# Optimization experiments

Measured on AMD Instinct MI355X. Metric: run time of the kernel, lower is better.

The kernel has to match this reference:

```python
import jax, jax.numpy as jnp
import numpy as np

I = 512   # input_size
H = 512   # hidden_size
Z = 0.1   # zoneout rate (eval-mode deterministic blend)
S = 128   # number of segments
B = 64    # batch


def setup_inputs() -> dict:
    rng = np.random.default_rng(0)
    durs = rng.integers(4, 13, size=(S, B)).astype(np.int64)  # [S, B], all >= 1
    T = int(durs.sum(0).max())
    key = jax.random.key(0)
    k0, k1, k2, k3, k4 = jax.random.split(key, 5)
    k = 1.0 / np.sqrt(H)
    x = jax.random.normal(k0, (T, B, I), jnp.float32)
    W_ih = jax.random.uniform(k1, (4 * H, I), jnp.float32, -k, k)
    W_hh = jax.random.uniform(k2, (4 * H, H), jnp.float32, -k, k)
    b_ih = jax.random.uniform(k3, (4 * H,), jnp.float32, -k, k)
    b_hh = jax.random.uniform(k4, (4 * H,), jnp.float32, -k, k)
    return {"x": x, "durs": jnp.asarray(durs), "W_ih": W_ih, "W_hh": W_hh,
            "b_ih": b_ih, "b_hh": b_hh}


def _duration_masks(durs, T):
    # durs: [S, B] -> per-batch segment-end (reset) frame indices and masks
    durs_bs = durs.T                                   # [B, S]
    reset_idx = jnp.cumsum(durs_bs, axis=1) - 1        # [B, S] last frame of each segment
    mel_lengths = jnp.sum(durs_bs, axis=1)             # [B]
    t = jnp.arange(T)
    reset_mask = jnp.any(t[None, :, None] == reset_idx[:, None, :], axis=-1)  # [B, T]
    valid = t[None, :] < mel_lengths[:, None]          # [B, T] frames within mel length
    retain = (~reset_mask) & valid                     # state kept where not reset/pad
    return reset_idx, retain.T, valid.T                # retain/valid as [T, B]


def reference(x, durs, W_ih, W_hh, b_ih, b_hh):
    T, Bb, _ = x.shape
    reset_idx, retain, valid = _duration_masks(durs, T)
    # Precompute the input contribution to the gates for all timesteps (one big GEMM)
    xg = jnp.einsum('tbi,gi->tbg', x, W_ih) + b_ih + b_hh   # [T, B, 4H]
    retain_f = retain.astype(x.dtype)                       # [T, B]

    def step(carry, inp):
        h, c = carry
        xg_t, retain_t = inp
        gates = xg_t + h @ W_hh.T                           # [B, 4H]
        i, f, g, o = jnp.split(gates, 4, axis=-1)           # torch LSTMCell order i,f,g,o
        i = jax.nn.sigmoid(i); f = jax.nn.sigmoid(f); o = jax.nn.sigmoid(o)
        g = jnp.tanh(g)
        c_new = f * c + i * g
        h_new = o * jnp.tanh(c_new)
        # eval-mode zoneout: deterministic blend with previous state
        h_z = Z * h + (1.0 - Z) * h_new
        c_z = Z * c + (1.0 - Z) * c_new
        m = retain_t[:, None]                               # zero state at segment resets / padding
        return (h_z * m, c_z * m), h_z

    h0 = jnp.zeros((Bb, H), x.dtype)
    (h, c), outputs = jax.lax.scan(step, (h0, h0), (xg, retain_f))
    outputs = outputs * valid[:, :, None].astype(outputs.dtype)  # [T, B, H]
    # segout: hidden state at each segment's last frame -> [B, S, H]
    segout = jnp.take_along_axis(outputs.transpose(1, 0, 2), reset_idx[:, :, None], axis=1)
    return outputs, h, c, segout
```

## Files before the change

kernel.cpp:

```cpp
#include <hip/hip_runtime.h>
#include <hip/hip_fp16.h>

#define IDIM 512
#define HDIM 512
#define NGATE 2048
#define SEGS 128
#define BATCH 64
#define ZK 0.1f

typedef _Float16 f16;
typedef _Float16 f16x8 __attribute__((ext_vector_type(8)));
typedef float f32x4 __attribute__((ext_vector_type(4)));

__device__ __forceinline__ void gload16(const void* g, void* l) {
  __builtin_amdgcn_global_load_lds((const __attribute__((address_space(1))) void*)g,
                                   (__attribute__((address_space(3))) void*)l, 16, 0, 0);
}
__device__ __forceinline__ float sigmoidf_(float x) { return 1.0f / (1.0f + __expf(-x)); }
__device__ __forceinline__ float tanhf_(float x) { return 2.0f / (1.0f + __expf(-2.0f * x)) - 1.0f; }

__global__ void prep_kernel(const int* __restrict__ durs, int4* __restrict__ meta,
                            int* __restrict__ Mk, int* __restrict__ mel) {
  __shared__ int hist[16];
  __shared__ int cur[16];
  int tid = threadIdx.x;
  if (tid < 16) hist[tid] = 0;
  __syncthreads();
  int b = tid;
  for (int s = 0; s < SEGS; ++s) {
    int d = durs[s * BATCH + b] & 15;
    atomicAdd(&hist[d], 1);
  }
  __syncthreads();
  if (tid == 0) {
    int run = 0;
    for (int d = 15; d >= 0; --d) { cur[d] = run; run += hist[d]; }
    for (int kk = 0; kk < 12; ++kk) Mk[kk] = cur[kk];
  }
  __syncthreads();
  int run = 0;
  for (int s = 0; s < SEGS; ++s) {
    int d = durs[s * BATCH + b] & 15;
    int pos = atomicAdd(&cur[d], 1);
    meta[pos] = make_int4(run, b, s, d);
    run += d;
  }
  mel[b] = run;
}

__global__ void wprep_kernel(const float* __restrict__ Wih, const float* __restrict__ Whh,
                             const float* __restrict__ bih, const float* __restrict__ bhh,
                             f16* __restrict__ Wc, float* __restrict__ biasp) {
  int n = blockIdx.x;
  int G = n >> 6, q = (n >> 4) & 3, r = n & 15;
  int j = G * 16 + r;
  int orig = q * 512 + j;
  for (int kk = threadIdx.x; kk < 1024; kk += blockDim.x) {
    float v = (kk < 512) ? Wih[(size_t)orig * 512 + kk] : Whh[(size_t)orig * 512 + kk - 512];
    Wc[(size_t)n * 1024 + kk] = (f16)v;
  }
  if (threadIdx.x == 0) biasp[n] = bih[orig] + bhh[orig];
}

__global__ void xconv_kernel(const float* __restrict__ x, f16* __restrict__ xh, long n8) {
  long i = (long)blockIdx.x * blockDim.x + threadIdx.x;
  long stride = (long)gridDim.x * blockDim.x;
  for (; i < n8; i += stride) {
    const float4* p = (const float4*)(x + i * 8);
    float4 a = p[0], bv = p[1];
    f16x8 o;
    o[0] = (f16)a.x;  o[1] = (f16)a.y;  o[2] = (f16)a.z;  o[3] = (f16)a.w;
    o[4] = (f16)bv.x; o[5] = (f16)bv.y; o[6] = (f16)bv.z; o[7] = (f16)bv.w;
    *(f16x8*)(xh + i * 8) = o;
  }
}

__global__ void zero_kernel(float* __restrict__ out, const int* __restrict__ mel, int T) {
  int bid = blockIdx.x;
  int tb = T * BATCH;
  if (bid < tb) {
    int t = bid / BATCH, b = bid - t * BATCH;
    if (t < mel[b]) return;
    float4* p = (float4*)(out + (size_t)bid * HDIM);
    p[threadIdx.x] = make_float4(0.f, 0.f, 0.f, 0.f);
  } else {
    int e = bid - tb;
    float4* p = (float4*)(out + (size_t)tb * HDIM + (size_t)e * HDIM);
    p[threadIdx.x] = make_float4(0.f, 0.f, 0.f, 0.f);
  }
}

template <bool FIRST>
__global__ __launch_bounds__(512, 1)
void step256_kernel(const f16* __restrict__ xh, const f16* __restrict__ Wc,
                    const float* __restrict__ biasp,
                    const f16* __restrict__ hprev, f16* __restrict__ hnext,
                    float* __restrict__ cst,
                    const int4* __restrict__ meta, const int* __restrict__ Mk,
                    float* __restrict__ out, int T, int k) {
  const int mk = Mk[k];
  const int nbx = gridDim.x;
  const int nwg = nbx * gridDim.y;
  const int orig = blockIdx.y * nbx + blockIdx.x;
  const int cpx = nwg >> 3;
  const int swz = (orig & 7) * cpx + (orig >> 3);
  const int by = swz / nbx, bx = swz - by * nbx;
  const int m0 = by * 256;
  if (m0 >= mk) return;
  const int n0 = bx * 256;

  __shared__ __align__(16) f16 As[2][256][64];
  __shared__ __align__(16) f16 Bs[2][256][64];
  __shared__ int4 metaS[256];

  const int tid = threadIdx.x;
  const int lane = tid & 63;
  const int w = tid >> 6;
  const int wr = w >> 2;
  const int wc = w & 3;
  const int lr = lane & 15;
  const int lk = lane >> 4;

  if (tid < 256) metaS[tid] = meta[m0 + tid];

  const int swzc = (((lane & 7) ^ ((lane >> 3) & 7)) << 3);
  size_t xoff[4];
  int ra4[4];
#pragma unroll
  for (int o = 0; o < 4; ++o) {
    int trow = o * 64 + w * 8 + (lane >> 3);
    int r = m0 + trow;
    int ra = (r < mk) ? r : 0;
    int4 mt = meta[ra];
    xoff[o] = ((size_t)(mt.x + k) * BATCH + mt.y) * IDIM + swzc;
    ra4[o] = ra;
  }

  auto stageA = [&](int o, int kb, int slot) {
    const f16* src;
    if (FIRST || kb < 8) src = xh + xoff[o] + kb * 64;
    else src = hprev + (size_t)ra4[o] * HDIM + (kb - 8) * 64 + swzc;
    gload16(src, &As[slot][o * 64 + w * 8][0]);
  };
  auto stageB = [&](int o, int kb, int slot) {
    int trow = o * 64 + w * 8 + (lane >> 3);
    gload16(Wc + (size_t)(n0 + trow) * 1024 + (size_t)kb * 64 + swzc,
            &Bs[slot][o * 64 + w * 8][0]);
  };
  auto stageOp = [&](int idx, int kb, int slot) {
    if (idx < 4) stageA(idx, kb, slot);
    else stageB(idx - 4, kb, slot);
  };

  auto lda = [&](int slot, int h, int f, int ks) -> f16x8 {
    int row = wr * 128 + h * 64 + f * 16 + lr;
    int ch = (((ks * 4 + lk) ^ (lr & 7)) << 3);
    return *(const f16x8*)&As[slot][row][ch];
  };
  auto ldb = [&](int slot, int q, int ks) -> f16x8 {
    int row = wc * 64 + q * 16 + lr;
    int ch = (((ks * 4 + lk) ^ (lr & 7)) << 3);
    return *(const f16x8*)&Bs[slot][row][ch];
  };

  f32x4 acc[8][4];
#pragma unroll
  for (int a = 0; a < 8; ++a)
#pragma unroll
    for (int bb = 0; bb < 4; ++bb) acc[a][bb] = (f32x4){0.f, 0.f, 0.f, 0.f};

#pragma unroll
  for (int idx = 0; idx < 8; ++idx) stageOp(idx, 0, 0);
  asm volatile("s_waitcnt vmcnt(0)" ::: "memory");
  __builtin_amdgcn_s_barrier();

  const int KB = FIRST ? 8 : 16;
  f16x8 aF[4][2], bF[4][2];

  for (int kt = 0; kt < KB; ++kt) {
    const int s = kt & 1;
    const int sn = s ^ 1;
    const int kn = kt + 1;
    const bool st = (kn < KB);

#pragma unroll
    for (int f = 0; f < 4; ++f)
#pragma unroll
      for (int ks = 0; ks < 2; ++ks) aF[f][ks] = lda(s, 0, f, ks);
#pragma unroll
    for (int q = 0; q < 4; ++q)
#pragma unroll
      for (int ks = 0; ks < 2; ++ks) bF[q][ks] = ldb(s, q, ks);
    if (st) { stageOp(0, kn, sn); stageOp(1, kn, sn); stageOp(2, kn, sn); }
    __builtin_amdgcn_s_barrier();
    __builtin_amdgcn_s_setprio(1);
#pragma unroll
    for (int f = 0; f < 4; ++f)
#pragma unroll
      for (int fn = 0; fn < 2; ++fn)
#pragma unroll
        for (int ks = 0; ks < 2; ++ks)
          acc[f][fn] = __builtin_amdgcn_mfma_f32_16x16x32_f16(aF[f][ks], bF[fn][ks], acc[f][fn], 0, 0, 0);
    __builtin_amdgcn_s_setprio(0);
    __builtin_amdgcn_s_barrier();

    if (st) { stageOp(3, kn, sn); stageOp(4, kn, sn); stageOp(5, kn, sn); }
    __builtin_amdgcn_s_barrier();
    __builtin_amdgcn_s_setprio(1);
#pragma unroll
    for (int f = 0; f < 4; ++f)
#pragma unroll
      for (int fn = 2; fn < 4; ++fn)
#pragma unroll
        for (int ks = 0; ks < 2; ++ks)
          acc[f][fn] = __builtin_amdgcn_mfma_f32_16x16x32_f16(aF[f][ks], bF[fn][ks], acc[f][fn], 0, 0, 0);
    __builtin_amdgcn_s_setprio(0);
    __builtin_amdgcn_s_barrier();

#pragma unroll
    for (int f = 0; f < 4; ++f)
#pragma unroll
      for (int ks = 0; ks < 2; ++ks) aF[f][ks] = lda(s, 1, f, ks);
    if (st) { stageOp(6, kn, sn); stageOp(7, kn, sn); }
    __builtin_amdgcn_s_barrier();
    __builtin_amdgcn_s_setprio(1);
#pragma unroll
    for (int f = 0; f < 4; ++f)
#pragma unroll
      for (int fn = 0; fn < 2; ++fn)
#pragma unroll
        for (int ks = 0; ks < 2; ++ks)
          acc[4 + f][fn] = __builtin_amdgcn_mfma_f32_16x16x32_f16(aF[f][ks], bF[fn][ks], acc[4 + f][fn], 0, 0, 0);
    __builtin_amdgcn_s_setprio(0);
    __builtin_amdgcn_s_barrier();

    __builtin_amdgcn_s_setprio(1);
#pragma unroll
    for (int f = 0; f < 4; ++f)
#pragma unroll
      for (int fn = 2; fn < 4; ++fn)
#pragma unroll
        for (int ks = 0; ks < 2; ++ks)
          acc[4 + f][fn] = __builtin_amdgcn_mfma_f32_16x16x32_f16(aF[f][ks], bF[fn][ks], acc[4 + f][fn], 0, 0, 0);
    __builtin_amdgcn_s_setprio(0);
    asm volatile("s_waitcnt vmcnt(0)" ::: "memory");
    __builtin_amdgcn_s_barrier();
  }

  float bq[4];
#pragma unroll
  for (int q = 0; q < 4; ++q) bq[q] = biasp[n0 + wc * 64 + q * 16 + lr];
  const int j = ((n0 + wc * 64) >> 6) * 16 + lr;
  const size_t segoff = (size_t)T * BATCH * HDIM + (size_t)2 * BATCH * HDIM;

#pragma unroll
  for (int fm = 0; fm < 8; ++fm) {
#pragma unroll
    for (int reg = 0; reg < 4; ++reg) {
      int m = m0 + wr * 128 + fm * 16 + ((lane >> 4) << 2) + reg;
      if (m >= mk) continue;
      int4 mt = metaS[m - m0];
      float gi = acc[fm][0][reg] + bq[0];
      float gf = acc[fm][1][reg] + bq[1];
      float gg = acc[fm][2][reg] + bq[2];
      float go = acc[fm][3][reg] + bq[3];
      float iv = sigmoidf_(gi), fv = sigmoidf_(gf);
      float gv = tanhf_(gg), ov = sigmoidf_(go);
      float cp, hp;
      if (FIRST) { cp = 0.f; hp = 0.f; }
      else {
        cp = cst[(size_t)m * HDIM + j];
        hp = (float)hprev[(size_t)m * HDIM + j];
      }
      float cn = fv * cp + iv * gv;
      float hn = ov * tanhf_(cn);
      float hz = ZK * hp + (1.f - ZK) * hn;
      float cz = ZK * cp + (1.f - ZK) * cn;
      out[((size_t)(mt.x + k) * BATCH + mt.y) * HDIM + j] = hz;
      if (k == mt.w - 1) {
        out[segoff + ((size_t)mt.y * SEGS + mt.z) * HDIM + j] = hz;
      } else {
        hnext[(size_t)m * HDIM + j] = (f16)hz;
        cst[(size_t)m * HDIM + j] = cz;
      }
    }
  }
}

template <bool FIRST>
__global__ void step_kernel(const f16* __restrict__ xh, const f16* __restrict__ Wc,
                            const float* __restrict__ biasp,
                            const f16* __restrict__ hprev, f16* __restrict__ hnext,
                            float* __restrict__ cst,
                            const int4* __restrict__ meta, const int* __restrict__ Mk,
                            float* __restrict__ out, int T, int k) {
  const int mk = Mk[k];
  const int m0 = blockIdx.y * 128;
  if (m0 >= mk) return;
  const int n0 = blockIdx.x * 128;

  __shared__ __align__(16) f16 At[128][64];
  __shared__ __align__(16) f16 Bt[128][64];
  __shared__ int4 metaS[128];

  const int tid = threadIdx.x;
  const int lane = tid & 63;
  const int w = tid >> 6;
  const int wr = w >> 1, wc = w & 1;

  if (tid < 128) metaS[tid] = meta[m0 + tid];

  const f16* xsrc[4];
  const f16* hsrc[4];
  const f16* wsrc[4];
#pragma unroll
  for (int i = 0; i < 4; ++i) {
    int r = m0 + w * 32 + i * 8 + (lane >> 3);
    int ra = (r < mk) ? r : 0;
    int4 mt = meta[ra];
    xsrc[i] = xh + ((size_t)(mt.x + k) * BATCH + mt.y) * IDIM;
    hsrc[i] = hprev + (size_t)ra * HDIM;
    wsrc[i] = Wc + (size_t)(n0 + w * 32 + i * 8 + (lane >> 3)) * 1024;
  }
  const int koff = (lane & 7) * 8;

  f32x4 acc[4][4];
#pragma unroll
  for (int a = 0; a < 4; ++a)
#pragma unroll
    for (int bb = 0; bb < 4; ++bb) acc[a][bb] = (f32x4){0.f, 0.f, 0.f, 0.f};

  const int KB = FIRST ? 8 : 16;
  for (int kb = 0; kb < KB; ++kb) {
    __syncthreads();
#pragma unroll
    for (int i = 0; i < 4; ++i) {
      const f16* s;
      if (FIRST) s = xsrc[i] + kb * 64 + koff;
      else       s = (kb < 8) ? (xsrc[i] + kb * 64 + koff) : (hsrc[i] + (kb - 8) * 64 + koff);
      gload16(s, &At[w * 32 + i * 8][0]);
    }
#pragma unroll
    for (int i = 0; i < 4; ++i) gload16(wsrc[i] + kb * 64 + koff, &Bt[w * 32 + i * 8][0]);
    __syncthreads();

    const int lr = lane & 15;
    const int lk = (lane >> 4) * 8;
#pragma unroll
    for (int ks = 0; ks < 2; ++ks) {
      f16x8 af[4], bfr[4];
#pragma unroll
      for (int f = 0; f < 4; ++f) af[f] = *(const f16x8*)&At[wr * 64 + f * 16 + lr][ks * 32 + lk];
#pragma unroll
      for (int f = 0; f < 4; ++f) bfr[f] = *(const f16x8*)&Bt[wc * 64 + f * 16 + lr][ks * 32 + lk];
#pragma unroll
      for (int fm = 0; fm < 4; ++fm)
#pragma unroll
        for (int fn = 0; fn < 4; ++fn)
          acc[fm][fn] = __builtin_amdgcn_mfma_f32_16x16x32_f16(af[fm], bfr[fn], acc[fm][fn], 0, 0, 0);
    }
  }

  const int r15 = lane & 15;
  float bq[4];
#pragma unroll
  for (int q = 0; q < 4; ++q) bq[q] = biasp[n0 + wc * 64 + q * 16 + r15];
  const int j = ((n0 + wc * 64) >> 6) * 16 + r15;
  const size_t segoff = (size_t)T * BATCH * HDIM + (size_t)2 * BATCH * HDIM;

#pragma unroll
  for (int fm = 0; fm < 4; ++fm) {
#pragma unroll
    for (int reg = 0; reg < 4; ++reg) {
      int m = m0 + wr * 64 + fm * 16 + ((lane >> 4) << 2) + reg;
      if (m >= mk) continue;
      int4 mt = metaS[m - m0];
      float gi = acc[fm][0][reg] + bq[0];
      float gf = acc[fm][1][reg] + bq[1];
      float gg = acc[fm][2][reg] + bq[2];
      float go = acc[fm][3][reg] + bq[3];
      float iv = sigmoidf_(gi), fv = sigmoidf_(gf);
      float gv = tanhf_(gg), ov = sigmoidf_(go);
      float cp, hp;
      if (FIRST) { cp = 0.f; hp = 0.f; }
      else {
        cp = cst[(size_t)m * HDIM + j];
        hp = (float)hprev[(size_t)m * HDIM + j];
      }
      float cn = fv * cp + iv * gv;
      float hn = ov * tanhf_(cn);
      float hz = ZK * hp + (1.f - ZK) * hn;
      float cz = ZK * cp + (1.f - ZK) * cn;
      out[((size_t)(mt.x + k) * BATCH + mt.y) * HDIM + j] = hz;
      if (k == mt.w - 1) {
        out[segoff + ((size_t)mt.y * SEGS + mt.z) * HDIM + j] = hz;
      } else {
        hnext[(size_t)m * HDIM + j] = (f16)hz;
        cst[(size_t)m * HDIM + j] = cz;
      }
    }
  }
}

extern "C" void kernel_launch(void* const* d_in, const int* in_sizes, int n_in,
                              void* d_out, int out_size, void* d_ws, size_t ws_size,
                              hipStream_t stream) {
  const float* x = (const float*)d_in[0];
  const int* durs = (const int*)d_in[1];
  const float* Wih = (const float*)d_in[2];
  const float* Whh = (const float*)d_in[3];
  const float* bih = (const float*)d_in[4];
  const float* bhh = (const float*)d_in[5];
  float* out = (float*)d_out;
  const int T = in_sizes[0] / (BATCH * IDIM);

  char* ws = (char*)d_ws;
  size_t off = 0;
  auto alloc = [&](size_t bytes) {
    void* p = ws + off;
    off = (off + bytes + 255) & ~(size_t)255;
    return p;
  };
  f16* xh     = (f16*)alloc((size_t)T * BATCH * IDIM * 2);
  f16* Wc     = (f16*)alloc((size_t)NGATE * 1024 * 2);
  float* biasp= (float*)alloc((size_t)NGATE * 4);
  f16* hst0   = (f16*)alloc((size_t)SEGS * BATCH * HDIM * 2);
  f16* hst1   = (f16*)alloc((size_t)SEGS * BATCH * HDIM * 2);
  float* cst  = (float*)alloc((size_t)SEGS * BATCH * HDIM * 4);
  int4* meta  = (int4*)alloc((size_t)SEGS * BATCH * 16);
  int* Mk     = (int*)alloc(64);
  int* mel    = (int*)alloc(64);

  prep_kernel<<<1, 64, 0, stream>>>(durs, meta, Mk, mel);
  wprep_kernel<<<NGATE, 256, 0, stream>>>(Wih, Whh, bih, bhh, Wc, biasp);
  long n8 = (long)T * BATCH * IDIM / 8;
  xconv_kernel<<<2048, 256, 0, stream>>>(x, xh, n8);
  zero_kernel<<<T * BATCH + 128, 128, 0, stream>>>(out, mel, T);

  dim3 hgrid(8, 32);
  step256_kernel<true><<<hgrid, 512, 0, stream>>>(xh, Wc, biasp, hst0, hst1, cst, meta, Mk, out, T, 0);
  for (int k = 1; k < 8; ++k) {
    f16* hp = (k & 1) ? hst1 : hst0;
    f16* hn = (k & 1) ? hst0 : hst1;
    step256_kernel<false><<<hgrid, 512, 0, stream>>>(xh, Wc, biasp, hp, hn, cst, meta, Mk, out, T, k);
  }
  dim3 sgrid(16, 64);
  for (int k = 8; k < 12; ++k) {
    f16* hp = (k & 1) ? hst1 : hst0;
    f16* hn = (k & 1) ? hst0 : hst1;
    step_kernel<false><<<sgrid, 256, 0, stream>>>(xh, Wc, biasp, hp, hn, cst, meta, Mk, out, T, k);
  }
}
```

Baseline: 650.1 us.

## Prefetch GEMM operand tiles two k-steps ahead in the double-buffered LDS

The A (input/hidden) and B (weight) tile loads are now issued two k-iterations ahead instead of one. The prologue stages two tiles, and each loop iteration writes the k+2 tile into the LDS slot just consumed, at points after the needed fragments have been read into registers. The wait becomes vmcnt(8) instead of a full drain, so one stage of global-to-LDS traffic stays in flight across the barrier and more load latency is hidden behind MFMA work. This relies on careful ordering of slot reuse against fragment reads, and a mistake there would silently corrupt the tiles.

```diff
diff --git a/kernel.cpp b/kernel.cpp
--- a/kernel.cpp
+++ b/kernel.cpp
@@ -147,10 +147,6 @@
     gload16(Wc + (size_t)(n0 + trow) * 1024 + (size_t)kb * 64 + swzc,
             &Bs[slot][o * 64 + w * 8][0]);
   };
-  auto stageOp = [&](int idx, int kb, int slot) {
-    if (idx < 4) stageA(idx, kb, slot);
-    else stageB(idx - 4, kb, slot);
-  };
 
   auto lda = [&](int slot, int h, int f, int ks) -> f16x8 {
     int row = wr * 128 + h * 64 + f * 16 + lr;
@@ -169,19 +165,25 @@
 #pragma unroll
     for (int bb = 0; bb < 4; ++bb) acc[a][bb] = (f32x4){0.f, 0.f, 0.f, 0.f};
 
-#pragma unroll
-  for (int idx = 0; idx < 8; ++idx) stageOp(idx, 0, 0);
-  asm volatile("s_waitcnt vmcnt(0)" ::: "memory");
+  const int KB = FIRST ? 8 : 16;
+
+#pragma unroll
+  for (int o = 0; o < 4; ++o) stageA(o, 0, 0);
+#pragma unroll
+  for (int o = 0; o < 4; ++o) stageB(o, 0, 0);
+#pragma unroll
+  for (int o = 0; o < 4; ++o) stageA(o, 1, 1);
+#pragma unroll
+  for (int o = 0; o < 4; ++o) stageB(o, 1, 1);
+  asm volatile("s_waitcnt vmcnt(8)" ::: "memory");
   __builtin_amdgcn_s_barrier();
 
-  const int KB = FIRST ? 8 : 16;
   f16x8 aF[4][2], bF[4][2];
 
   for (int kt = 0; kt < KB; ++kt) {
     const int s = kt & 1;
-    const int sn = s ^ 1;
-    const int kn = kt + 1;
-    const bool st = (kn < KB);
+    const bool st1 = (kt + 1 < KB);
+    const bool st2 = (kt + 2 < KB);
 
 #pragma unroll
     for (int f = 0; f < 4; ++f)
@@ -191,7 +193,6 @@
     for (int q = 0; q < 4; ++q)
 #pragma unroll
       for (int ks = 0; ks < 2; ++ks) bF[q][ks] = ldb(s, q, ks);
-    if (st) { stageOp(0, kn, sn); stageOp(1, kn, sn); stageOp(2, kn, sn); }
     __builtin_amdgcn_s_barrier();
     __builtin_amdgcn_s_setprio(1);
 #pragma unroll
@@ -204,7 +205,10 @@
     __builtin_amdgcn_s_setprio(0);
     __builtin_amdgcn_s_barrier();
 
-    if (st) { stageOp(3, kn, sn); stageOp(4, kn, sn); stageOp(5, kn, sn); }
+    if (st2) {
+#pragma unroll
+      for (int o = 0; o < 4; ++o) stageB(o, kt + 2, s);
+    }
     __builtin_amdgcn_s_barrier();
     __builtin_amdgcn_s_setprio(1);
 #pragma unroll
@@ -221,7 +225,7 @@
     for (int f = 0; f < 4; ++f)
 #pragma unroll
       for (int ks = 0; ks < 2; ++ks) aF[f][ks] = lda(s, 1, f, ks);
-    if (st) { stageOp(6, kn, sn); stageOp(7, kn, sn); }
+    if (st2) { stageA(0, kt + 2, s); stageA(2, kt + 2, s); }
     __builtin_amdgcn_s_barrier();
     __builtin_amdgcn_s_setprio(1);
 #pragma unroll
@@ -234,6 +238,7 @@
     __builtin_amdgcn_s_setprio(0);
     __builtin_amdgcn_s_barrier();
 
+    if (st2) { stageA(1, kt + 2, s); stageA(3, kt + 2, s); }
     __builtin_amdgcn_s_setprio(1);
 #pragma unroll
     for (int f = 0; f < 4; ++f)
@@ -243,7 +248,11 @@
         for (int ks = 0; ks < 2; ++ks)
           acc[4 + f][fn] = __builtin_amdgcn_mfma_f32_16x16x32_f16(aF[f][ks], bF[fn][ks], acc[4 + f][fn], 0, 0, 0);
     __builtin_amdgcn_s_setprio(0);
-    asm volatile("s_waitcnt vmcnt(0)" ::: "memory");
+    if (st2) {
+      asm volatile("s_waitcnt vmcnt(8)" ::: "memory");
+    } else if (st1) {
+      asm volatile("s_waitcnt vmcnt(0)" ::: "memory");
+    }
     __builtin_amdgcn_s_barrier();
   }
 
```

After: 654.7 us. No clear change (+0.7%).
